# Optimization experiments

Hardware: AMD Instinct MI355X
Metric: run time of the kernel (lower is better)

The kernel has to match this reference:

```python
import jax, jax.numpy as jnp
import numpy as np
import math

L = 16
F = 2
T = 2 ** 19  # hashmap size (power of two)
BASE_RES = 16
MAX_RES = 2048
GROWTH = math.exp((math.log(MAX_RES) - math.log(BASE_RES)) / (L - 1))
RESOLUTIONS = np.array([int(math.ceil(BASE_RES * GROWTH ** l)) for l in range(L)], dtype=np.float32)
PRIMES = np.array([1, 2654435761, 805459861], dtype=np.uint32)
# 8 corner offsets of a unit cube, ordered as in the torch module
OFFSETS = np.array([[0,0,0],[0,0,1],[0,1,0],[0,1,1],[1,0,0],[1,0,1],[1,1,0],[1,1,1]], dtype=np.int32)
BBOX_MIN, BBOX_MAX = -1.0, 1.0


def setup_inputs() -> dict:
    key = jax.random.key(0)
    k1, k2 = jax.random.split(key)
    N = 1_000_000
    # world-space positions uniformly inside the default bbox [-1, 1]^3
    positions = jax.random.uniform(k1, (N, 3), dtype=jnp.float32, minval=-1.0, maxval=1.0)
    # hash tables init: uniform(-1e-4, 1e-4), matching nn.init.uniform_
    hash_tables = jax.random.uniform(k2, (L, T, F), dtype=jnp.float32, minval=-1e-4, maxval=1e-4)
    return {"positions": positions, "hash_tables": hash_tables}


def _hash_grid_forward(positions, hash_tables):
    res = jnp.asarray(RESOLUTIONS)                      # [L]
    primes = jnp.asarray(PRIMES)                        # [3] uint32
    offsets = jnp.asarray(OFFSETS)                      # [8,3] int32

    normalized = (positions - BBOX_MIN) / (BBOX_MAX - BBOX_MIN + 1e-8)
    normalized = jnp.clip(normalized, 0.0, 1.0 - 1e-6)  # [N,3]
    scaled = normalized[:, None, :] * res[None, :, None]  # [N,L,3]
    floor_coords = jnp.floor(scaled).astype(jnp.int32)
    frac = scaled - floor_coords.astype(jnp.float32)      # [N,L,3]

    corners = floor_coords[:, :, None, :] + offsets[None, None, :, :]  # [N,L,8,3]
    # spatial hash: (x*p0 ^ y*p1 ^ z*p2) mod T; uint32 wrap-around is
    # equivalent to the int64 torch version modulo T since T | 2^32
    c = corners.astype(jnp.uint32)
    h = (c[..., 0] * primes[0]) ^ (c[..., 1] * primes[1]) ^ (c[..., 2] * primes[2])
    hash_idx = (h % jnp.uint32(T)).astype(jnp.int32)      # [N,L,8]

    level_off = (jnp.arange(L, dtype=jnp.int32) * T)[None, :, None]  # [1,L,1]
    flat_idx = level_off + hash_idx                        # [N,L,8]
    corner_feats = hash_tables.reshape(L * T, F)[flat_idx]  # [N,L,8,F]

    fx = frac[..., 0:1]  # [N,L,1]
    fy = frac[..., 1:2]
    fz = frac[..., 2:3]
    c00 = corner_feats[:, :, 0] * (1 - fz) + corner_feats[:, :, 1] * fz
    c01 = corner_feats[:, :, 2] * (1 - fz) + corner_feats[:, :, 3] * fz
    c10 = corner_feats[:, :, 4] * (1 - fz) + corner_feats[:, :, 5] * fz
    c11 = corner_feats[:, :, 6] * (1 - fz) + corner_feats[:, :, 7] * fz
    c0 = c00 * (1 - fy) + c01 * fy
    c1 = c10 * (1 - fy) + c11 * fy
    out = c0 * (1 - fx) + c1 * fx                          # [N,L,F]
    return out.reshape(positions.shape[0], L * F)


def reference(positions, hash_tables):
    return _hash_grid_forward(positions, hash_tables)
```

## Files before the change

### kernel.cpp

```cpp
#include <hip/hip_runtime.h>
#include <math.h>

#define NUM_LEVELS 16
#define T_SIZE (1u << 19)
#define T_MASK (T_SIZE - 1u)
#define PRIME1 2654435761u
#define PRIME2 805459861u

struct ResParams { float r[NUM_LEVELS]; };

typedef float f32x2 __attribute__((ext_vector_type(2)));
typedef float f32x4 __attribute__((ext_vector_type(4)));

__device__ __forceinline__ void nt_store_f2(float2 v, float2* p) {
    f32x2 x; x.x = v.x; x.y = v.y;
    __builtin_nontemporal_store(x, (f32x2*)p);
}
__device__ __forceinline__ float2 nt_load_f2(const float2* p) {
    f32x2 x = __builtin_nontemporal_load((const f32x2*)p);
    float2 r; r.x = x.x; r.y = x.y; return r;
}
__device__ __forceinline__ void nt_store_f4(f32x4 v, float* p) {
    __builtin_nontemporal_store(v, (f32x4*)p);
}
__device__ __forceinline__ f32x4 nt_load_f4(const float* p) {
    return __builtin_nontemporal_load((const f32x4*)p);
}

struct CornerSet {
    unsigned idx[8];
    unsigned ux;
    float fx, fy, fz;
};

__device__ __forceinline__ void calc_corners(
    float px, float py, float pz, float res, unsigned base, CornerSet& cs)
{
    float nx = (px + 1.0f) * 0.5f;
    float ny = (py + 1.0f) * 0.5f;
    float nz = (pz + 1.0f) * 0.5f;
    const float HI = 0.999999f;
    nx = fminf(fmaxf(nx, 0.0f), HI);
    ny = fminf(fmaxf(ny, 0.0f), HI);
    nz = fminf(fmaxf(nz, 0.0f), HI);

    float sx = nx * res, sy = ny * res, sz = nz * res;
    float flx = floorf(sx), fly = floorf(sy), flz = floorf(sz);
    cs.fx = sx - flx; cs.fy = sy - fly; cs.fz = sz - flz;

    unsigned ux = (unsigned)(int)flx;
    unsigned uy = (unsigned)(int)fly;
    unsigned uz = (unsigned)(int)flz;
    cs.ux = ux;

    unsigned hx0 = ux;            unsigned hx1 = ux + 1u;
    unsigned hy0 = uy * PRIME1;   unsigned hy1 = hy0 + PRIME1;
    unsigned hz0 = uz * PRIME2;   unsigned hz1 = hz0 + PRIME2;

    cs.idx[0] = base + ((hx0 ^ hy0 ^ hz0) & T_MASK);
    cs.idx[1] = base + ((hx0 ^ hy0 ^ hz1) & T_MASK);
    cs.idx[2] = base + ((hx0 ^ hy1 ^ hz0) & T_MASK);
    cs.idx[3] = base + ((hx0 ^ hy1 ^ hz1) & T_MASK);
    cs.idx[4] = base + ((hx1 ^ hy0 ^ hz0) & T_MASK);
    cs.idx[5] = base + ((hx1 ^ hy0 ^ hz1) & T_MASK);
    cs.idx[6] = base + ((hx1 ^ hy1 ^ hz0) & T_MASK);
    cs.idx[7] = base + ((hx1 ^ hy1 ^ hz1) & T_MASK);
}

__device__ __forceinline__ void load_feats(
    const float2* __restrict__ table, const CornerSet& cs, float2 f[8])
{
    const f32x4* t4 = reinterpret_cast<const f32x4*>(table);
#pragma unroll
    for (int j = 0; j < 4; ++j) {
        unsigned i0 = cs.idx[j];
        f32x4 v = t4[i0 >> 1];
        float2 lo; lo.x = v.x; lo.y = v.y;
        float2 hi; hi.x = v.z; hi.y = v.w;
        bool sw = (i0 & 1u) != 0u;
        f[j]     = sw ? hi : lo;
        f[4 + j] = sw ? lo : hi;
    }
    if (cs.ux & 1u) {
#pragma unroll
        for (int j = 0; j < 4; ++j) f[4 + j] = table[cs.idx[4 + j]];
    }
}

__device__ __forceinline__ float2 trilerp(const float2 f[8], float fx, float fy, float fz)
{
    float omz = 1.0f - fz, omy = 1.0f - fy, omx = 1.0f - fx;
    float c00x = f[0].x * omz + f[1].x * fz;
    float c00y = f[0].y * omz + f[1].y * fz;
    float c01x = f[2].x * omz + f[3].x * fz;
    float c01y = f[2].y * omz + f[3].y * fz;
    float c10x = f[4].x * omz + f[5].x * fz;
    float c10y = f[4].y * omz + f[5].y * fz;
    float c11x = f[6].x * omz + f[7].x * fz;
    float c11y = f[6].y * omz + f[7].y * fz;
    float c0x = c00x * omy + c01x * fy;
    float c0y = c00y * omy + c01y * fy;
    float c1x = c10x * omy + c11x * fy;
    float c1y = c10y * omy + c11y * fy;
    float2 o;
    o.x = c0x * omx + c1x * fx;
    o.y = c0y * omx + c1y * fx;
    return o;
}

__global__ __launch_bounds__(256) void hashgrid_gather_kernel(
    const float* __restrict__ pos,
    const float2* __restrict__ table,
    float2* __restrict__ ws,
    ResParams rp, int N)
{
    int level = blockIdx.y;
    int t = threadIdx.x;
    int n0 = blockIdx.x * 512 + 2 * t;
    int n1 = n0 + 1;
    bool v0 = n0 < N;
    bool v1 = n1 < N;
    if (!v0) return;

    float res = rp.r[level];
    unsigned base = (unsigned)level * T_SIZE;

    float px0 = pos[3 * n0 + 0], py0 = pos[3 * n0 + 1], pz0 = pos[3 * n0 + 2];
    int m1 = v1 ? n1 : n0;
    float px1 = pos[3 * m1 + 0], py1 = pos[3 * m1 + 1], pz1 = pos[3 * m1 + 2];

    CornerSet c0, c1;
    calc_corners(px0, py0, pz0, res, base, c0);
    calc_corners(px1, py1, pz1, res, base, c1);

    float2 f0[8], f1[8];
    load_feats(table, c0, f0);
    load_feats(table, c1, f1);

    float2 o0 = trilerp(f0, c0.fx, c0.fy, c0.fz);
    float2 o1 = trilerp(f1, c1.fx, c1.fy, c1.fz);

    size_t w = (size_t)level * N + n0;
    if (v1) {
        f32x4 v; v.x = o0.x; v.y = o0.y; v.z = o1.x; v.w = o1.y;
        nt_store_f4(v, (float*)&ws[w]);
    } else {
        nt_store_f2(o0, &ws[w]);
    }
}

__global__ __launch_bounds__(256) void hashgrid_untile_kernel(
    const float2* __restrict__ ws,
    float* __restrict__ out,
    int N)
{
    int g = blockIdx.x * 256 + threadIdx.x;
    int q = g >> 3;
    int m = g & 7;
    int p0 = 2 * q;
    if (p0 >= N) return;

    const float* wsf = (const float*)ws;
    if (p0 + 1 < N) {
        f32x4 a = nt_load_f4(&wsf[((size_t)(2 * m) * N + p0) * 2]);
        f32x4 b = nt_load_f4(&wsf[((size_t)(2 * m + 1) * N + p0) * 2]);
        f32x4 v0; v0.x = a.x; v0.y = a.y; v0.z = b.x; v0.w = b.y;
        f32x4 v1; v1.x = a.z; v1.y = a.w; v1.z = b.z; v1.w = b.w;
        nt_store_f4(v0, &out[(size_t)p0 * 32 + m * 4]);
        nt_store_f4(v1, &out[(size_t)(p0 + 1) * 32 + m * 4]);
    } else {
        float2 a = nt_load_f2(&ws[(size_t)(2 * m) * N + p0]);
        float2 b = nt_load_f2(&ws[(size_t)(2 * m + 1) * N + p0]);
        f32x4 v; v.x = a.x; v.y = a.y; v.z = b.x; v.w = b.y;
        nt_store_f4(v, &out[(size_t)p0 * 32 + m * 4]);
    }
}

__global__ __launch_bounds__(256) void hashgrid_fused_kernel(
    const float* __restrict__ pos,
    const float2* __restrict__ table,
    float2* __restrict__ out,
    ResParams rp, int N)
{
    int tid = blockIdx.x * blockDim.x + threadIdx.x;
    int n = tid >> 4;
    int l = tid & 15;
    if (n >= N) return;
    float px = pos[3 * n + 0], py = pos[3 * n + 1], pz = pos[3 * n + 2];
    CornerSet c;
    calc_corners(px, py, pz, rp.r[l], (unsigned)l * T_SIZE, c);
    float2 f[8];
    load_feats(table, c, f);
    out[tid] = trilerp(f, c.fx, c.fy, c.fz);
}

extern "C" void kernel_launch(void* const* d_in, const int* in_sizes, int n_in,
                              void* d_out, int out_size, void* d_ws, size_t ws_size,
                              hipStream_t stream) {
    const float*  pos   = (const float*)d_in[0];
    const float2* table = (const float2*)d_in[1];
    int N = in_sizes[0] / 3;

    ResParams rp;
    double growth = exp((log(2048.0) - log(16.0)) / 15.0);
    for (int l = 0; l < NUM_LEVELS; ++l) {
        rp.r[l] = (float)ceil(16.0 * pow(growth, (double)l));
    }

    size_t ws_needed = (size_t)NUM_LEVELS * (size_t)N * sizeof(float2);
    if (ws_size >= ws_needed) {
        float2* ws = (float2*)d_ws;
        int chunks = (N + 511) / 512;
        dim3 grid(chunks, NUM_LEVELS);
        hashgrid_gather_kernel<<<grid, 256, 0, stream>>>(pos, table, ws, rp, N);
        long long tthreads = ((long long)(N + 1) / 2) * 8;
        int tblocks = (int)((tthreads + 255) / 256);
        hashgrid_untile_kernel<<<tblocks, 256, 0, stream>>>(ws, (float*)d_out, N);
    } else {
        long long total = (long long)N * NUM_LEVELS;
        int grid = (int)((total + 255) / 256);
        hashgrid_fused_kernel<<<grid, 256, 0, stream>>>(pos, table, (float2*)d_out, rp, N);
    }
}
```

Baseline: 607.8 us.

## Stage low-resolution level grids in shared memory via dedicated kernel

Adds a separate kernel for the two coarsest levels (res 16 and 24). It precomputes the hashed feature for every grid vertex into LDS once per block, then does the trilinear lookups from LDS over 8192 points per block. The main gather kernel now covers only the remaining 14 levels. It also changes load_feats to take either the paired vector-load path or eight scalar loads when x is odd, and rewrites the fallback fused kernel to loop over levels per point. The intent is to cut redundant global gathers for the small levels, at the cost of an extra launch and a low-occupancy kernel (launch_bounds 256,1, 110KB shared memory for the 24^3 grid).

```diff
diff --git a/kernel.cpp b/kernel.cpp
--- a/kernel.cpp
+++ b/kernel.cpp
@@ -6,6 +6,10 @@
 #define T_MASK (T_SIZE - 1u)
 #define PRIME1 2654435761u
 #define PRIME2 805459861u
+
+#define LOW_LEVELS 2
+#define LOW_PTS 8192
+#define LOW_DIM 24
 
 struct ResParams { float r[NUM_LEVELS]; };
 
@@ -70,20 +74,21 @@
 __device__ __forceinline__ void load_feats(
     const float2* __restrict__ table, const CornerSet& cs, float2 f[8])
 {
-    const f32x4* t4 = reinterpret_cast<const f32x4*>(table);
+    if ((cs.ux & 1u) == 0u) {
+        const f32x4* t4 = reinterpret_cast<const f32x4*>(table);
 #pragma unroll
-    for (int j = 0; j < 4; ++j) {
-        unsigned i0 = cs.idx[j];
-        f32x4 v = t4[i0 >> 1];
-        float2 lo; lo.x = v.x; lo.y = v.y;
-        float2 hi; hi.x = v.z; hi.y = v.w;
-        bool sw = (i0 & 1u) != 0u;
-        f[j]     = sw ? hi : lo;
-        f[4 + j] = sw ? lo : hi;
-    }
-    if (cs.ux & 1u) {
+        for (int j = 0; j < 4; ++j) {
+            unsigned i0 = cs.idx[j];
+            f32x4 v = t4[i0 >> 1];
+            float2 lo; lo.x = v.x; lo.y = v.y;
+            float2 hi; hi.x = v.z; hi.y = v.w;
+            bool sw = (i0 & 1u) != 0u;
+            f[j]     = sw ? hi : lo;
+            f[4 + j] = sw ? lo : hi;
+        }
+    } else {
 #pragma unroll
-        for (int j = 0; j < 4; ++j) f[4 + j] = table[cs.idx[4 + j]];
+        for (int i = 0; i < 8; ++i) f[i] = table[cs.idx[i]];
     }
 }
 
@@ -108,13 +113,73 @@
     return o;
 }
 
+template<int R1>
+__device__ __forceinline__ void lowlevel_body(
+    const float* __restrict__ pos, const float2* __restrict__ table,
+    float2* __restrict__ ws, float res, int level, int N, float2* cell)
+{
+    const int R1sq = R1 * R1;
+    unsigned base = (unsigned)level * T_SIZE;
+
+    for (int s = threadIdx.x; s < R1 * R1sq; s += 256) {
+        int x = s / R1sq;
+        int r = s - x * R1sq;
+        int y = r / R1;
+        int z = r - y * R1;
+        unsigned h = ((unsigned)x ^ ((unsigned)y * PRIME1)
+                                  ^ ((unsigned)z * PRIME2)) & T_MASK;
+        cell[s] = table[base + h];
+    }
+    __syncthreads();
+
+    int start = blockIdx.x * LOW_PTS;
+    int end = start + LOW_PTS; if (end > N) end = N;
+    const float HI = 0.999999f;
+    for (int n = start + (int)threadIdx.x; n < end; n += 256) {
+        float px = pos[3 * n + 0], py = pos[3 * n + 1], pz = pos[3 * n + 2];
+        float nx = fminf(fmaxf((px + 1.0f) * 0.5f, 0.0f), HI);
+        float ny = fminf(fmaxf((py + 1.0f) * 0.5f, 0.0f), HI);
+        float nz = fminf(fmaxf((pz + 1.0f) * 0.5f, 0.0f), HI);
+        float sx = nx * res, sy = ny * res, sz = nz * res;
+        float flx = floorf(sx), fly = floorf(sy), flz = floorf(sz);
+        float fx = sx - flx, fy = sy - fly, fz = sz - flz;
+        int ix = (int)flx, iy = (int)fly, iz = (int)flz;
+        int i000 = (ix * R1 + iy) * R1 + iz;
+
+        float2 f[8];
+        f[0] = cell[i000];
+        f[1] = cell[i000 + 1];
+        f[2] = cell[i000 + R1];
+        f[3] = cell[i000 + R1 + 1];
+        f[4] = cell[i000 + R1sq];
+        f[5] = cell[i000 + R1sq + 1];
+        f[6] = cell[i000 + R1sq + R1];
+        f[7] = cell[i000 + R1sq + R1 + 1];
+
+        float2 o = trilerp(f, fx, fy, fz);
+        nt_store_f2(o, &ws[(size_t)level * N + n]);
+    }
+}
+
+__global__ __launch_bounds__(256, 1) void hashgrid_lowlevel_kernel(
+    const float* __restrict__ pos,
+    const float2* __restrict__ table,
+    float2* __restrict__ ws,
+    ResParams rp, int N)
+{
+    __shared__ float2 cell[LOW_DIM * LOW_DIM * LOW_DIM];
+    int level = blockIdx.y;
+    if (level == 0) lowlevel_body<17>(pos, table, ws, rp.r[0], 0, N, cell);
+    else            lowlevel_body<24>(pos, table, ws, rp.r[1], 1, N, cell);
+}
+
 __global__ __launch_bounds__(256) void hashgrid_gather_kernel(
     const float* __restrict__ pos,
     const float2* __restrict__ table,
     float2* __restrict__ ws,
     ResParams rp, int N)
 {
-    int level = blockIdx.y;
+    int level = blockIdx.y + LOW_LEVELS;
     int t = threadIdx.x;
     int n0 = blockIdx.x * 512 + 2 * t;
     int n1 = n0 + 1;
@@ -176,22 +241,33 @@
     }
 }
 
-__global__ __launch_bounds__(256) void hashgrid_fused_kernel(
+__global__ __launch_bounds__(256) void hashgrid_fused16_kernel(
     const float* __restrict__ pos,
     const float2* __restrict__ table,
-    float2* __restrict__ out,
+    float* __restrict__ out,
     ResParams rp, int N)
 {
-    int tid = blockIdx.x * blockDim.x + threadIdx.x;
-    int n = tid >> 4;
-    int l = tid & 15;
+    int n = blockIdx.x * 256 + threadIdx.x;
     if (n >= N) return;
     float px = pos[3 * n + 0], py = pos[3 * n + 1], pz = pos[3 * n + 2];
-    CornerSet c;
-    calc_corners(px, py, pz, rp.r[l], (unsigned)l * T_SIZE, c);
-    float2 f[8];
-    load_feats(table, c, f);
-    out[tid] = trilerp(f, c.fx, c.fy, c.fz);
+    const float HI = 0.999999f;
+    float nx = fminf(fmaxf((px + 1.0f) * 0.5f, 0.0f), HI);
+    float ny = fminf(fmaxf((py + 1.0f) * 0.5f, 0.0f), HI);
+    float nz = fminf(fmaxf((pz + 1.0f) * 0.5f, 0.0f), HI);
+    float* po = out + (size_t)n * 32;
+#pragma unroll 1
+    for (int pr = 0; pr < 8; ++pr) {
+        CornerSet c0, c1;
+        calc_corners(px, py, pz, rp.r[2 * pr],     (unsigned)(2 * pr) * T_SIZE, c0);
+        calc_corners(px, py, pz, rp.r[2 * pr + 1], (unsigned)(2 * pr + 1) * T_SIZE, c1);
+        float2 f0[8], f1[8];
+        load_feats(table, c0, f0);
+        load_feats(table, c1, f1);
+        float2 o0 = trilerp(f0, c0.fx, c0.fy, c0.fz);
+        float2 o1 = trilerp(f1, c1.fx, c1.fy, c1.fz);
+        f32x4 v; v.x = o0.x; v.y = o0.y; v.z = o1.x; v.w = o1.y;
+        *reinterpret_cast<f32x4*>(po + 4 * pr) = v;
+    }
 }
 
 extern "C" void kernel_launch(void* const* d_in, const int* in_sizes, int n_in,
@@ -210,15 +286,21 @@
     size_t ws_needed = (size_t)NUM_LEVELS * (size_t)N * sizeof(float2);
     if (ws_size >= ws_needed) {
         float2* ws = (float2*)d_ws;
+
+        int lowblocks = (N + LOW_PTS - 1) / LOW_PTS;
+        dim3 lgrid(lowblocks, LOW_LEVELS);
+        hashgrid_lowlevel_kernel<<<lgrid, 256, 0, stream>>>(pos, table, ws, rp, N);
+
         int chunks = (N + 511) / 512;
-        dim3 grid(chunks, NUM_LEVELS);
-        hashgrid_gather_kernel<<<grid, 256, 0, stream>>>(pos, table, ws, rp, N);
+        dim3 ggrid(chunks, NUM_LEVELS - LOW_LEVELS);
+        hashgrid_gather_kernel<<<ggrid, 256, 0, stream>>>(pos, table, ws, rp, N);
+
         long long tthreads = ((long long)(N + 1) / 2) * 8;
         int tblocks = (int)((tthreads + 255) / 256);
         hashgrid_untile_kernel<<<tblocks, 256, 0, stream>>>(ws, (float*)d_out, N);
     } else {
-        long long total = (long long)N * NUM_LEVELS;
-        int grid = (int)((total + 255) / 256);
-        hashgrid_fused_kernel<<<grid, 256, 0, stream>>>(pos, table, (float2*)d_out, rp, N);
-    }
-}
+        int fb = (N + 255) / 256;
+        hashgrid_fused16_kernel<<<fb, 256, 0, stream>>>(
+            pos, table, (float*)d_out, rp, N);
+    }
+}
```

Measured after the change: 559.9 us. -7.9%, faster.
